# Kernel tuning notes

Hardware: AMD Instinct MI355X
Metric: run time of the kernel (lower is better)

Reference implementation:

```python
import jax, jax.numpy as jnp
import numpy as np
from jax import lax

K = 3          # kernel size
PAD = 1        # (K-1)//2
C = 64         # channels
RED = 16       # channel-attention reduction


def conv2d(x, w, b=None):
    # x [B,C,H,W], w [O,I,kh,kw]
    out = lax.conv_general_dilated(x, w, (1, 1), 'SAME',
                                   dimension_numbers=('NCHW', 'OIHW', 'NCHW'))
    if b is not None:
        out = out + b[None, :, None, None]
    return out


def rcab(x, w1, b1, w2, b2, caw1, cab1, caw2, cab2):
    res = conv2d(x, w1, b1)
    res = jax.nn.relu(res)
    res = conv2d(res, w2, b2)
    # channel attention: global avg pool -> 1x1 conv -> relu -> 1x1 conv -> sigmoid
    y = jnp.mean(res, axis=(2, 3), keepdims=True)
    y = jax.nn.relu(conv2d(y, caw1, cab1))
    y = jax.nn.sigmoid(conv2d(y, caw2, cab2))
    return res * y + x


def deform_conv(x, inter, fea, off_w, off_b, mask_w, mask_b, weight):
    # Modulated deformable conv: offsets/mask predicted from concat(inter, fea).
    B, Cc, H, W = x.shape
    KK = K * K
    guide = jnp.concatenate([inter, fea], axis=1)
    offset = conv2d(guide, off_w, off_b)                    # [B, 2*KK, H, W]
    mask = 2.0 * jax.nn.sigmoid(conv2d(guide, mask_w, mask_b))  # [B, KK, H, W]
    off = offset.reshape(B, KK, 2, H, W)
    oy, ox = off[:, :, 0], off[:, :, 1]                     # [B, KK, H, W]

    ky = (jnp.arange(KK) // K - PAD).astype(x.dtype)        # kernel tap y offsets
    kx = (jnp.arange(KK) % K - PAD).astype(x.dtype)
    ii = jnp.arange(H, dtype=x.dtype)[None, None, :, None]
    jj = jnp.arange(W, dtype=x.dtype)[None, None, None, :]
    ys = ii + ky[None, :, None, None] + oy                  # [B, KK, H, W]
    xs = jj + kx[None, :, None, None] + ox

    y0 = jnp.floor(ys); x0 = jnp.floor(xs)
    wy1 = ys - y0; wy0 = 1.0 - wy1
    wx1 = xs - x0; wx0 = 1.0 - wx1
    y0i = y0.astype(jnp.int32); x0i = x0.astype(jnp.int32)
    y1i = y0i + 1; x1i = x0i + 1

    x_flat = x.reshape(B, Cc, H * W)

    def gather(yi, xi):
        valid = ((yi >= 0) & (yi < H) & (xi >= 0) & (xi < W)).astype(x.dtype)
        idx = jnp.clip(yi, 0, H - 1) * W + jnp.clip(xi, 0, W - 1)   # [B,KK,H,W]
        idx = idx.reshape(B, KK * H * W)
        g = jax.vmap(lambda f, i: jnp.take(f, i, axis=1))(x_flat, idx)
        return g.reshape(B, Cc, KK, H, W) * valid[:, None]

    val = (gather(y0i, x0i) * (wy0 * wx0)[:, None]
           + gather(y0i, x1i) * (wy0 * wx1)[:, None]
           + gather(y1i, x0i) * (wy1 * wx0)[:, None]
           + gather(y1i, x1i) * (wy1 * wx1)[:, None])     # [B,C,KK,H,W]
    val = val * mask[:, None]
    w_flat = weight.reshape(weight.shape[0], Cc, KK)        # [O,I,KK]
    return jnp.einsum('bckhw,ock->bohw', val, w_flat)


def setup_inputs() -> dict:
    key = jax.random.key(0)
    ks = jax.random.split(key, 20)
    B, H, W = 4, 192, 192
    f32 = jnp.float32
    d = {
        'x':     jax.random.normal(ks[0], (B, C, H, W), f32),
        'inter': jax.random.normal(ks[1], (B, C, H, W), f32),
        'fea':   jax.random.normal(ks[2], (B, C, H, W), f32),
        # RCAB
        'rcab_w1': jax.random.normal(ks[3], (C, C, 3, 3), f32) * 0.05,
        'rcab_b1': jnp.zeros((C,), f32),
        'rcab_w2': jax.random.normal(ks[4], (C, C, 3, 3), f32) * 0.05,
        'rcab_b2': jnp.zeros((C,), f32),
        'ca_w1': jax.random.normal(ks[5], (C // RED, C, 1, 1), f32) * 0.05,
        'ca_b1': jnp.zeros((C // RED,), f32),
        'ca_w2': jax.random.normal(ks[6], (C, C // RED, 1, 1), f32) * 0.05,
        'ca_b2': jnp.zeros((C,), f32),
        # deformable conv offset/mask branch (input = concat(inter, fea) -> 2C)
        'off_w': jax.random.normal(ks[7], (2 * K * K, 2 * C, 3, 3), f32) * 0.01,
        'off_b': jnp.zeros((2 * K * K,), f32),
        'mask_w': jax.random.normal(ks[8], (K * K, 2 * C, 3, 3), f32) * 0.01,
        'mask_b': jnp.zeros((K * K,), f32),
        'deform_w': jax.random.normal(ks[9], (C, C, K, K), f32) * 0.05,
        # final conv
        'conv_w': jax.random.normal(ks[10], (C, C, 3, 3), f32) * 0.05,
        'conv_b': jnp.zeros((C,), f32),
    }
    return d


def reference(x, inter, fea, rcab_w1, rcab_b1, rcab_w2, rcab_b2,
              ca_w1, ca_b1, ca_w2, ca_b2,
              off_w, off_b, mask_w, mask_b, deform_w, conv_w, conv_b):
    out1 = rcab(x, rcab_w1, rcab_b1, rcab_w2, rcab_b2, ca_w1, ca_b1, ca_w2, ca_b2)
    out2 = deform_conv(out1, inter, fea, off_w, off_b, mask_w, mask_b, deform_w)
    return conv2d(out2 + out1, conv_w, conv_b)
```

## Files before the change

kernel.cpp:

```cpp
#include <hip/hip_runtime.h>
#include <hip/hip_bf16.h>
#include <hip/hip_fp16.h>
#include <math.h>

#define HSZ 192
#define WSZ 192
#define HWSZ (192*192)
#define PH 194
#define PP (PH*PH)
#define NB 4

typedef __attribute__((ext_vector_type(8))) short short8;
typedef __attribute__((ext_vector_type(4))) float f32x4;
typedef __attribute__((ext_vector_type(2))) float f32x2;

__device__ inline unsigned short f2bf(float f) { __hip_bfloat16 h = __float2bfloat16(f); return *(unsigned short*)&h; }
__device__ inline float bf2f(__hip_bfloat16 h) { return __bfloat162float(h); }
__device__ inline float bflo(unsigned u) { return __uint_as_float(u << 16); }
__device__ inline float bfhi(unsigned u) { return __uint_as_float(u & 0xffff0000u); }
__device__ inline f32x2 up2(unsigned u) {
  f32x2 r; r[0] = __uint_as_float(u << 16); r[1] = __uint_as_float(u & 0xffff0000u); return r;
}

#define GLDS(SRC, DST) __builtin_amdgcn_global_load_lds( \
    (const __attribute__((address_space(1))) unsigned int*)(const void*)(SRC), \
    (__attribute__((address_space(3))) unsigned int*)(void*)(DST), 16, 0, 0)

#define MFMA(A,B,C) __builtin_amdgcn_mfma_f32_16x16x32_bf16((A),(B),(C),0,0,0)

__global__ void zb2_k(__hip_bfloat16* xn, __hip_bfloat16* r1, __hip_bfloat16* out1,
                      __hip_bfloat16* cat) {
  int job = blockIdx.y;
  __hip_bfloat16* buf = job == 0 ? xn : job == 1 ? r1 : job == 2 ? out1 : cat;
  int Cn = (job == 3) ? 128 : 64;
  int cg8 = Cn >> 3;
  int tot = NB * 772 * cg8;
  int idx = blockIdx.x * 256 + threadIdx.x;
  if (idx >= tot) return;
  int cg = idx % cg8; int rem = idx / cg8;
  int e = rem % 772; int b = rem / 772;
  int h, w2;
  if (e < 194) { h = 0; w2 = e; }
  else if (e < 388) { h = 193; w2 = e - 194; }
  else if (e < 580) { h = e - 388 + 1; w2 = 0; }
  else { h = e - 580 + 1; w2 = 193; }
  uint4 z = make_uint4(0, 0, 0, 0);
  *(uint4*)&buf[(((size_t)b * PH + h) * PH + w2) * Cn + cg * 8] = z;
}

__global__ void wts_k(const float* __restrict__ rw1, const float* __restrict__ rw2,
                      const float* __restrict__ cw, const float* __restrict__ offw,
                      const float* __restrict__ maskw, const float* __restrict__ offb,
                      const float* __restrict__ maskb, const float* __restrict__ dwv,
                      short* wt1, short* wt2c, short* wtf, short* wtom, float* ob,
                      short* wtb, float* meanz) {
  int job = blockIdx.y;
  int idx = blockIdx.x * 256 + threadIdx.x;
  if (job < 3) {
    const float* src = job == 0 ? rw1 : job == 1 ? rw2 : cw;
    short* dst = job == 0 ? wt1 : job == 1 ? wt2c : wtf;
    int kk = idx >> 12, rem = idx & 4095;
    int co = rem >> 6, ci = rem & 63;
    dst[idx] = (short)f2bf(src[(co * 64 + ci) * 9 + kk]);
  } else if (job == 3) {
    int kk = idx >> 12, rem = idx & 4095;
    int co = rem >> 7, ci = rem & 127;
    float v = 0.f;
    if (co < 18) v = offw[(co * 128 + ci) * 9 + kk];
    else if (co < 27) v = maskw[((co - 18) * 128 + ci) * 9 + kk];
    wtom[idx] = (short)f2bf(v);
    if (idx < 32) ob[idx] = idx < 18 ? offb[idx] : (idx < 27 ? maskb[idx - 18] : 0.f);
  } else {
    int o = idx / 576, rem = idx - o * 576;
    int kk = rem >> 6, ci = rem & 63;
    wtb[idx] = (short)f2bf(dwv[(o * 64 + ci) * 9 + kk]);
    if (blockIdx.x == 0 && threadIdx.x < 256) meanz[threadIdx.x] = 0.f;
  }
}

__global__ __launch_bounds__(256) void cvt_k(const float* __restrict__ x,
    const float* __restrict__ inter, const float* __restrict__ fea,
    __hip_bfloat16* __restrict__ xn, __hip_bfloat16* __restrict__ cat) {
  int job = blockIdx.z;
  const float* src = job == 0 ? x : job == 1 ? inter : fea;
  __hip_bfloat16* dst = job == 0 ? xn : cat;
  int Cdst = job == 0 ? 64 : 128;
  int coff = job == 2 ? 64 : 0;
  __shared__ float s[64][65];
  int p0 = blockIdx.x * 64; int b = blockIdx.y;
  int lane = threadIdx.x & 63, g = threadIdx.x >> 6;
#pragma unroll
  for (int i = 0; i < 16; ++i) {
    int c = i * 4 + g;
    s[c][lane] = src[((size_t)b * 64 + c) * HWSZ + p0 + lane];
  }
  __syncthreads();
  int pix = threadIdx.x >> 2, cg = threadIdx.x & 3;
  int h = p0 / WSZ, w0 = p0 - h * WSZ + pix;
  size_t addr = (((size_t)b * PH + h + 1) * PH + 1 + w0) * Cdst + coff + cg * 16;
  unsigned pk2[8];
#pragma unroll
  for (int t = 0; t < 8; ++t)
    pk2[t] = (unsigned)f2bf(s[cg * 16 + 2 * t][pix]) | ((unsigned)f2bf(s[cg * 16 + 2 * t + 1][pix]) << 16);
  *(uint4*)&dst[addr]     = make_uint4(pk2[0], pk2[1], pk2[2], pk2[3]);
  *(uint4*)&dst[addr + 8] = make_uint4(pk2[4], pk2[5], pk2[6], pk2[7]);
}

template<int OUT_MODE, bool RELU, bool MEANACC>
__global__ __launch_bounds__(256, 2) void conv_mfma_k(
    const __hip_bfloat16* __restrict__ inp, const short* __restrict__ wt,
    const float* __restrict__ bias, __hip_bfloat16* __restrict__ outB,
    float* __restrict__ outF, float* __restrict__ meanout) {
  int flat = (blockIdx.x & 7) * 96 + (blockIdx.x >> 3);
  const int b = flat / 192, h = flat - (flat / 192) * 192;
  const int tid = threadIdx.x, lane = tid & 63, wid = tid >> 6;
  const int q = lane >> 4, r16 = lane & 15;
  __shared__ __align__(16) short tile[3 * 200 * 64];
  __shared__ float smean[4][64];

  {
    const char* gb = (const char*)(inp + ((size_t)b * PH + h) * (PH * 64));
    for (int s = wid; s < 75; s += 4) {
      int rr = s / 25, si = s - rr * 25;
      int pix = 8 * si + (lane >> 3);
      const char* src = gb + (size_t)rr * (PH * 128) + pix * 128
                      + ((((lane & 7) ^ ((lane >> 3) & 7))) << 4);
      GLDS(src, tile + rr * 12800 + si * 512);
    }
  }

  f32x4 acc[3][4];
  if (OUT_MODE == 0) {
#pragma unroll
    for (int nf = 0; nf < 4; ++nf) {
      float4 bv = *(const float4*)&bias[nf * 16 + q * 4];
      f32x4 v; v[0] = bv.x; v[1] = bv.y; v[2] = bv.z; v[3] = bv.w;
      acc[0][nf] = v; acc[1][nf] = v; acc[2][nf] = v;
    }
  } else {
#pragma unroll
    for (int nf = 0; nf < 4; ++nf) {
      float bs = bias[nf * 16 + r16];
      f32x4 v; v[0] = bs; v[1] = bs; v[2] = bs; v[3] = bs;
      acc[0][nf] = v; acc[1][nf] = v; acc[2][nf] = v;
    }
  }

  short8 bfr[2][2][4];
  {
    const short* wk0 = wt + r16 * 64 + q * 8;
#pragma unroll
    for (int nf = 0; nf < 4; ++nf) {
      bfr[0][0][nf] = *(const short8*)(wk0 + nf * 1024);
      bfr[0][1][nf] = *(const short8*)(wk0 + nf * 1024 + 32);
    }
  }
  __syncthreads();

  const int wm0 = wid * 48;
#pragma unroll
  for (int kk = 0; kk < 9; ++kk) {
    const int ky = kk / 3, kx = kk - ky * 3;
    const int cur = kk & 1;
    if (kk < 8) {
      const short* wk = wt + (kk + 1) * 4096 + r16 * 64 + q * 8;
#pragma unroll
      for (int nf = 0; nf < 4; ++nf) {
        bfr[cur ^ 1][0][nf] = *(const short8*)(wk + nf * 1024);
        bfr[cur ^ 1][1][nf] = *(const short8*)(wk + nf * 1024 + 32);
      }
    }
#pragma unroll
    for (int mf = 0; mf < 3; ++mf) {
      int pix = wm0 + mf * 16 + r16 + kx;
      const char* ab = (const char*)tile + ky * 25600 + pix * 128;
      int sw = (pix & 7) << 4;
      short8 a0 = *(const short8*)(ab + ((q << 4) ^ sw));
      short8 a1 = *(const short8*)(ab + (((q + 4) << 4) ^ sw));
#pragma unroll
      for (int nf = 0; nf < 4; ++nf) {
        if (OUT_MODE == 0) {
          acc[mf][nf] = MFMA(bfr[cur][0][nf], a0, acc[mf][nf]);
          acc[mf][nf] = MFMA(bfr[cur][1][nf], a1, acc[mf][nf]);
        } else {
          acc[mf][nf] = MFMA(a0, bfr[cur][0][nf], acc[mf][nf]);
          acc[mf][nf] = MFMA(a1, bfr[cur][1][nf], acc[mf][nf]);
        }
      }
    }
  }

  if (MEANACC) {
    float t[4][4];
#pragma unroll
    for (int nf = 0; nf < 4; ++nf)
#pragma unroll
      for (int rg = 0; rg < 4; ++rg)
        t[nf][rg] = acc[0][nf][rg] + acc[1][nf][rg] + acc[2][nf][rg];
#pragma unroll
    for (int m = 1; m < 16; m <<= 1)
#pragma unroll
      for (int nf = 0; nf < 4; ++nf)
#pragma unroll
        for (int rg = 0; rg < 4; ++rg)
          t[nf][rg] += __shfl_xor(t[nf][rg], m);
    if (r16 == 0)
#pragma unroll
      for (int nf = 0; nf < 4; ++nf)
#pragma unroll
        for (int rg = 0; rg < 4; ++rg)
          smean[wid][nf * 16 + q * 4 + rg] = t[nf][rg];
    __syncthreads();
    if (tid < 64)
      atomicAdd(&meanout[b * 64 + tid],
                (smean[0][tid] + smean[1][tid] + smean[2][tid] + smean[3][tid]) * (1.f / 36864.f));
  }

  if (OUT_MODE == 0) {
    __syncthreads();
#pragma unroll
    for (int mf = 0; mf < 3; ++mf)
#pragma unroll
      for (int nf = 0; nf < 4; ++nf) {
        f32x4 v = acc[mf][nf];
        if (RELU) { v[0] = fmaxf(v[0], 0.f); v[1] = fmaxf(v[1], 0.f); v[2] = fmaxf(v[2], 0.f); v[3] = fmaxf(v[3], 0.f); }
        unsigned lo = (unsigned)f2bf(v[0]) | ((unsigned)f2bf(v[1]) << 16);
        unsigned hi = (unsigned)f2bf(v[2]) | ((unsigned)f2bf(v[3]) << 16);
        int pix = wm0 + mf * 16 + r16;
        int byteoff = (pix * 128 + nf * 32 + q * 8) ^ ((pix & 7) << 4);
        *(uint2*)((char*)tile + byteoff) = make_uint2(lo, hi);
      }
    __syncthreads();
    char* orow = (char*)outB + ((((size_t)b * PH + h + 1) * PH + 1) * 64) * 2;
    for (int s = wid; s < 24; s += 4) {
      int pix = 8 * s + (lane >> 3);
      int g16 = ((lane & 7) ^ (pix & 7)) << 4;
      uint4 d = *(const uint4*)((const char*)tile + pix * 128 + g16);
      *(uint4*)(orow + pix * 128 + ((lane & 7) << 4)) = d;
    }
  } else {
    float* ob2 = outF + (size_t)b * 64 * HWSZ + h * WSZ;
#pragma unroll
    for (int mf = 0; mf < 3; ++mf)
#pragma unroll
      for (int nf = 0; nf < 4; ++nf) {
        int pix0 = wm0 + mf * 16 + q * 4;
        int co = nf * 16 + r16;
        *(f32x4*)&ob2[(size_t)co * HWSZ + pix0] = acc[mf][nf];
      }
  }
}

__global__ __launch_bounds__(256, 3) void offmask_mfma_k(
    const __hip_bfloat16* __restrict__ cat, const short* __restrict__ wt2,
    const float* __restrict__ ob, float* __restrict__ om) {
  const int h = blockIdx.x, b = blockIdx.y;
  const int tid = threadIdx.x, lane = tid & 63, wid = tid >> 6;
  const int q = lane >> 4, r16 = lane & 15;
  __shared__ __align__(16) short tile[200 * 128];

  f32x4 acc[3][2];
#pragma unroll
  for (int nf = 0; nf < 2; ++nf) {
    float bs = ob[nf * 16 + r16];
    f32x4 v; v[0] = bs; v[1] = bs; v[2] = bs; v[3] = bs;
    acc[0][nf] = v; acc[1][nf] = v; acc[2][nf] = v;
  }
  const char* gb = (const char*)(cat + ((size_t)b * PH + h) * (PH * 128));
  const int wm0 = wid * 48;

  short8 bfr[2][4][2];
  {
    const short* wk0 = wt2 + r16 * 128 + q * 8;
#pragma unroll
    for (int c4 = 0; c4 < 4; ++c4) {
      bfr[0][c4][0] = *(const short8*)(wk0 + c4 * 32);
      bfr[0][c4][1] = *(const short8*)(wk0 + 2048 + c4 * 32);
    }
  }

#pragma unroll
  for (int r = 0; r < 3; ++r) {
    __syncthreads();
    for (int s = wid; s < 50; s += 4) {
      int pix = 4 * s + (lane >> 4);
      const char* src = gb + (size_t)r * (PH * 256) + pix * 256
                      + ((((lane & 15) ^ (pix & 15))) << 4);
      GLDS(src, tile + s * 512);
    }
    __syncthreads();
#pragma unroll
    for (int kx = 0; kx < 3; ++kx) {
      const int kk = r * 3 + kx;
      const int cur = kk & 1;
      if (kk < 8) {
        const short* wk = wt2 + (kk + 1) * 4096 + r16 * 128 + q * 8;
#pragma unroll
        for (int c4 = 0; c4 < 4; ++c4) {
          bfr[cur ^ 1][c4][0] = *(const short8*)(wk + c4 * 32);
          bfr[cur ^ 1][c4][1] = *(const short8*)(wk + 2048 + c4 * 32);
        }
      }
#pragma unroll
      for (int mf = 0; mf < 3; ++mf) {
        int pix = wm0 + mf * 16 + r16 + kx;
        const char* ab = (const char*)tile + pix * 256;
        int sw = (pix & 15) << 4;
        short8 a0 = *(const short8*)(ab + ((q << 4) ^ sw));
        short8 a1 = *(const short8*)(ab + (((4 + q) << 4) ^ sw));
        short8 a2 = *(const short8*)(ab + (((8 + q) << 4) ^ sw));
        short8 a3 = *(const short8*)(ab + (((12 + q) << 4) ^ sw));
        acc[mf][0] = MFMA(a0, bfr[cur][0][0], acc[mf][0]); acc[mf][1] = MFMA(a0, bfr[cur][0][1], acc[mf][1]);
        acc[mf][0] = MFMA(a1, bfr[cur][1][0], acc[mf][0]); acc[mf][1] = MFMA(a1, bfr[cur][1][1], acc[mf][1]);
        acc[mf][0] = MFMA(a2, bfr[cur][2][0], acc[mf][0]); acc[mf][1] = MFMA(a2, bfr[cur][2][1], acc[mf][1]);
        acc[mf][0] = MFMA(a3, bfr[cur][3][0], acc[mf][0]); acc[mf][1] = MFMA(a3, bfr[cur][3][1], acc[mf][1]);
      }
    }
  }
#pragma unroll
  for (int mf = 0; mf < 3; ++mf)
#pragma unroll
    for (int nf = 0; nf < 2; ++nf) {
      int co = nf * 16 + r16;
      if (co < 27) {
        f32x4 v = acc[mf][nf];
        if (co >= 18) {
          v[0] = 2.f / (1.f + expf(-v[0])); v[1] = 2.f / (1.f + expf(-v[1]));
          v[2] = 2.f / (1.f + expf(-v[2])); v[3] = 2.f / (1.f + expf(-v[3]));
        }
        *(f32x4*)&om[((size_t)(b * 27 + co)) * HWSZ + h * WSZ + wm0 + mf * 16 + q * 4] = v;
      }
    }
}

__global__ __launch_bounds__(256) void out1_k(const __hip_bfloat16* __restrict__ res, const __hip_bfloat16* __restrict__ xn,
    const float* __restrict__ mean, const float* __restrict__ w1, const float* __restrict__ b1,
    const float* __restrict__ w2, const float* __restrict__ b2,
    __hip_bfloat16* __restrict__ out1) {
  int idx = blockIdx.x * 256 + threadIdx.x;
  int b = idx / 294912; int rem = idx - b * 294912;
  int p = rem >> 3, c8 = rem & 7;
  int lane = threadIdx.x & 63, wid = threadIdx.x >> 6;

  __shared__ float s_t[4];
  {
    float prod = w1[wid * 64 + lane] * mean[b * 64 + lane];
#pragma unroll
    for (int m = 1; m < 64; m <<= 1) prod += __shfl_xor(prod, m);
    if (lane == 0) s_t[wid] = fmaxf(prod + b1[wid], 0.f);
  }
  __syncthreads();
  float t0 = s_t[0], t1 = s_t[1], t2 = s_t[2], t3 = s_t[3];

  int hh = p / WSZ, ww = p - hh * WSZ;
  size_t off = ((size_t)b * PP + (size_t)(hh + 1) * PH + ww + 1) * 64 + c8 * 8;
  const __hip_bfloat16* rp = res + off;
  const __hip_bfloat16* xp = xn + off;
  __hip_bfloat16* op = out1 + off;
  unsigned pk[4];
#pragma unroll
  for (int t = 0; t < 4; ++t) {
    float y0, y1;
    {
      int c = c8 * 8 + 2 * t;
      const float4 wv0 = *(const float4*)&w2[c * 4];
      const float4 wv1 = *(const float4*)&w2[(c + 1) * 4];
      float v0 = b2[c]     + wv0.x * t0 + wv0.y * t1 + wv0.z * t2 + wv0.w * t3;
      float v1 = b2[c + 1] + wv1.x * t0 + wv1.y * t1 + wv1.z * t2 + wv1.w * t3;
      y0 = 1.f / (1.f + expf(-v0));
      y1 = 1.f / (1.f + expf(-v1));
    }
    float o0 = bf2f(rp[2 * t]) * y0 + bf2f(xp[2 * t]);
    float o1 = bf2f(rp[2 * t + 1]) * y1 + bf2f(xp[2 * t + 1]);
    pk[t] = (unsigned)f2bf(o0) | ((unsigned)f2bf(o1) << 16);
  }
  *(uint4*)op = make_uint4(pk[0], pk[1], pk[2], pk[3]);
}

__global__ __launch_bounds__(256) void deform_mfma_k(
    const __hip_bfloat16* __restrict__ nhwc, const float* __restrict__ om,
    const short* __restrict__ wtb, __hip_bfloat16* __restrict__ fin) {
  int blk = (blockIdx.x & 7) * 576 + (blockIdx.x >> 3);
  int b = blk / 1152;
  int p0 = (blk - b * 1152) * 32;
  int tid = threadIdx.x, lane = tid & 63, wid = tid >> 6;
  int q = lane >> 4, r16 = lane & 15;
  __shared__ __align__(16) short sA[2][32][64];
  __shared__ __half2 s_bw[2][9][32];
  __shared__ int s_pk[9][32];

  const float* omb = om + (size_t)b * 27 * HWSZ + p0;
  for (int e = tid; e < 288; e += 256) {
    int kk = e >> 5, pix = e & 31;
    int p = p0 + pix;
    int h = p / WSZ, w2 = p - h * WSZ;
    float oy = omb[(size_t)(2 * kk) * HWSZ + pix];
    float ox = omb[(size_t)(2 * kk + 1) * HWSZ + pix];
    float m2 = omb[(size_t)(18 + kk) * HWSZ + pix];
    float ys = (float)(h + kk / 3 - 1) + oy;
    float xs = (float)(w2 + kk % 3 - 1) + ox;
    float y0f = floorf(ys), x0f = floorf(xs);
    float wy1 = ys - y0f, wx1 = xs - x0f;
    float wy0 = 1.f - wy1, wx0 = 1.f - wx1;
    int y0 = (int)y0f, x0i = (int)x0f;
    int y1 = y0 + 1, x1 = x0i + 1;
    float vy0 = (y0 >= 0 && y0 < HSZ) ? 1.f : 0.f;
    float vx0 = (x0i >= 0 && x0i < WSZ) ? 1.f : 0.f;
    float vy1 = (y1 >= 0 && y1 < HSZ) ? 1.f : 0.f;
    float vx1 = (x1 >= 0 && x1 < WSZ) ? 1.f : 0.f;
    int y0c = min(max(y0, 0), HSZ - 1), x0c = min(max(x0i, 0), WSZ - 1);
    int y1c = min(max(y1, 0), HSZ - 1), x1c = min(max(x1, 0), WSZ - 1);
    s_bw[0][kk][pix] = __floats2half2_rn(wy0 * wx0 * m2 * vy0 * vx0, wy0 * wx1 * m2 * vy0 * vx1);
    s_bw[1][kk][pix] = __floats2half2_rn(wy1 * wx0 * m2 * vy1 * vx0, wy1 * wx1 * m2 * vy1 * vx1);
    s_pk[kk][pix] = ((((y0c + 1) * PH) + x0c + 1) << 2) | ((y1c - y0c) << 1) | (x1c - x0c);
  }
  __syncthreads();

  const __hip_bfloat16* nb = nhwc + (size_t)b * PP * 64;
  const int spix = tid >> 3, lg = tid & 7;
  const int swz = (spix & 7) << 4;
  const int rsw = (r16 & 7) << 4;

  uint4 A0, B0, C0, D0, A1, B1, C1, D1, A2, B2, C2, D2;
  float2 wab0, wcd0, wab1, wcd1, wab2, wcd2;

#define ISSUE_R(KK, Av, Bv, Cv, Dv, Wab, Wcd) do { \
    Wab = __half22float2(s_bw[0][KK][spix]); \
    Wcd = __half22float2(s_bw[1][KK][spix]); \
    int pk_ = s_pk[KK][spix]; \
    int i00_ = pk_ >> 2, dy_ = (pk_ >> 1) & 1, dx_ = pk_ & 1; \
    const __hip_bfloat16* g_ = nb + (size_t)i00_ * 64 + lg * 8; \
    Av = *(const uint4*)g_; \
    Bv = *(const uint4*)(g_ + dx_ * 64); \
    Cv = *(const uint4*)(g_ + dy_ * (PH * 64)); \
    Dv = *(const uint4*)(g_ + (dy_ * PH + dx_) * 64); \
  } while (0)
#define CSTORE_R(BUFOFF, Av, Bv, Cv, Dv, Wab, Wcd) do { \
    const unsigned* ap_ = (const unsigned*)&Av; const unsigned* bp_ = (const unsigned*)&Bv; \
    const unsigned* cp_ = (const unsigned*)&Cv; const unsigned* dp_ = (const unsigned*)&Dv; \
    unsigned o_[4]; \
    _Pragma("unroll") \
    for (int j_ = 0; j_ < 4; ++j_) { \
      f32x2 v_ = up2(ap_[j_]) * Wab.x + up2(bp_[j_]) * Wab.y + up2(cp_[j_]) * Wcd.x + up2(dp_[j_]) * Wcd.y; \
      asm("v_cvt_pk_bf16_f32 %0, %1, %2" : "=v"(o_[j_]) : "v"(v_[0]), "v"(v_[1])); \
    } \
    *(uint4*)((char*)sA + (BUFOFF) + spix * 128 + ((lg * 16) ^ swz)) = make_uint4(o_[0], o_[1], o_[2], o_[3]); \
  } while (0)

  ISSUE_R(0, A0, B0, C0, D0, wab0, wcd0);
  CSTORE_R(0, A0, B0, C0, D0, wab0, wcd0);
  ISSUE_R(1, A0, B0, C0, D0, wab0, wcd0);
  ISSUE_R(2, A1, B1, C1, D1, wab1, wcd1);
  ISSUE_R(3, A2, B2, C2, D2, wab2, wcd2);

  f32x4 acc0 = (f32x4){0.f, 0.f, 0.f, 0.f};
  f32x4 acc1 = (f32x4){0.f, 0.f, 0.f, 0.f};
  const short* wrow = wtb + (size_t)(wid * 16 + r16) * 576;
  const char* a0base = (const char*)sA + r16 * 128;
  const char* a1base = (const char*)sA + (r16 + 16) * 128;

#pragma unroll
  for (int kk = 0; kk < 9; ++kk) {
    const int bo = (kk & 1) * 4096;
    __syncthreads();
    __builtin_amdgcn_s_setprio(1);
#pragma unroll
    for (int s = 0; s < 2; ++s) {
      short8 wf = *(const short8*)(wrow + kk * 64 + s * 32 + q * 8);
      int off = bo + ((s * 64 + q * 16) ^ rsw);
      short8 va = *(const short8*)(a0base + off);
      short8 vb = *(const short8*)(a1base + off);
      acc0 = MFMA(wf, va, acc0);
      acc1 = MFMA(wf, vb, acc1);
    }
    __builtin_amdgcn_s_setprio(0);
    if (kk < 8) {
      const int nbo = ((kk + 1) & 1) * 4096;
      const int rs = kk % 3;
      if (rs == 0) {
        CSTORE_R(nbo, A0, B0, C0, D0, wab0, wcd0);
        if (kk + 4 <= 8) ISSUE_R(kk + 4, A0, B0, C0, D0, wab0, wcd0);
      } else if (rs == 1) {
        CSTORE_R(nbo, A1, B1, C1, D1, wab1, wcd1);
        if (kk + 4 <= 8) ISSUE_R(kk + 4, A1, B1, C1, D1, wab1, wcd1);
      } else {
        CSTORE_R(nbo, A2, B2, C2, D2, wab2, wcd2);
        if (kk + 4 <= 8) ISSUE_R(kk + 4, A2, B2, C2, D2, wab2, wcd2);
      }
    }
  }

  int h0 = p0 / WSZ, w0 = p0 - h0 * WSZ;
  size_t ro = ((size_t)(h0 + 1) * PH + w0 + 1) * 64;
  const __hip_bfloat16* resid = nb + ro;
  __hip_bfloat16* fp = fin + (size_t)b * PP * 64 + ro;
#pragma unroll
  for (int nf = 0; nf < 2; ++nf) {
    f32x4 av = nf ? acc1 : acc0;
    int pix = r16 + nf * 16;
    int co = wid * 16 + q * 4;
    const unsigned* rr = (const unsigned*)(resid + (size_t)pix * 64 + co);
    unsigned r0 = rr[0], r1 = rr[1];
    float o0 = av[0] + bflo(r0);
    float o1 = av[1] + bfhi(r0);
    float o2 = av[2] + bflo(r1);
    float o3 = av[3] + bfhi(r1);
    uint2 pk2 = make_uint2((unsigned)f2bf(o0) | ((unsigned)f2bf(o1) << 16),
                           (unsigned)f2bf(o2) | ((unsigned)f2bf(o3) << 16));
    *(uint2*)(fp + (size_t)pix * 64 + co) = pk2;
  }
#undef ISSUE_R
#undef CSTORE_R
}

extern "C" void kernel_launch(void* const* d_in, const int* in_sizes, int n_in,
                              void* d_out, int out_size, void* d_ws, size_t ws_size,
                              hipStream_t stream) {
  (void)in_sizes; (void)n_in; (void)out_size; (void)ws_size;
  const float* x     = (const float*)d_in[0];
  const float* inter = (const float*)d_in[1];
  const float* fea   = (const float*)d_in[2];
  const float* rw1   = (const float*)d_in[3];
  const float* rb1   = (const float*)d_in[4];
  const float* rw2   = (const float*)d_in[5];
  const float* rb2   = (const float*)d_in[6];
  const float* caw1  = (const float*)d_in[7];
  const float* cab1  = (const float*)d_in[8];
  const float* caw2  = (const float*)d_in[9];
  const float* cab2  = (const float*)d_in[10];
  const float* offw  = (const float*)d_in[11];
  const float* offb  = (const float*)d_in[12];
  const float* maskw = (const float*)d_in[13];
  const float* maskb = (const float*)d_in[14];
  const float* dw    = (const float*)d_in[15];
  const float* cw    = (const float*)d_in[16];
  const float* cb    = (const float*)d_in[17];

  char* w = (char*)d_ws;
  const size_t P64 = (size_t)NB * PP * 64 * 2 + 4096;
  const size_t PCAT = (size_t)NB * PP * 128 * 2 + 4096;
  __hip_bfloat16* xn   = (__hip_bfloat16*)(w);
  __hip_bfloat16* r1   = (__hip_bfloat16*)(w + P64);
  __hip_bfloat16* res  = (__hip_bfloat16*)(w + 2 * P64);
  __hip_bfloat16* out1 = (__hip_bfloat16*)(w + 3 * P64);
  __hip_bfloat16* cat  = (__hip_bfloat16*)(w + 4 * P64);
  char* tail = w + 4 * P64 + PCAT;
  short* wt1  = (short*)tail; tail += 73728;
  short* wt2c = (short*)tail; tail += 73728;
  short* wtf  = (short*)tail; tail += 73728;
  short* wtom = (short*)tail; tail += 73728;
  float* obb  = (float*)tail; tail += 128;
  short* wtb  = (short*)tail; tail += 73728;
  float* mean = (float*)tail; tail += 1024;
  float* omb  = (float*)res;
  __hip_bfloat16* fin = r1;

  zb2_k<<<dim3(194, 4), 256, 0, stream>>>(xn, r1, out1, cat);
  wts_k<<<dim3(144, 5), 256, 0, stream>>>(rw1, rw2, cw, offw, maskw, offb, maskb, dw,
                                          wt1, wt2c, wtf, wtom, obb, wtb, mean);
  cvt_k<<<dim3(576, 4, 3), 256, 0, stream>>>(x, inter, fea, xn, cat);

  conv_mfma_k<0, true , false><<<768, 256, 0, stream>>>(xn, wt1, rb1, r1, nullptr, nullptr);
  conv_mfma_k<0, false, true ><<<768, 256, 0, stream>>>(r1, wt2c, rb2, res, nullptr, mean);
  out1_k<<<4608, 256, 0, stream>>>(res, xn, mean, caw1, cab1, caw2, cab2, out1);
  offmask_mfma_k<<<dim3(192, 4), 256, 0, stream>>>(cat, wtom, obb, omb);
  deform_mfma_k<<<NB * 1152, 256, 0, stream>>>(out1, omb, wtb, fin);
  conv_mfma_k<1, false, false><<<768, 256, 0, stream>>>(fin, wtf, cb, nullptr, (float*)d_out, nullptr);
}
```

Before: 272.5 us.

## Double-buffer conv input rows in LDS and raise conv occupancy

The 3x3 conv kernel now stages one padded input row at a time into two ping-pong LDS buffers instead of loading all three rows up front. It loads the next row while MFMAs run on the current one. This cuts LDS per block from three rows to two, so launch bounds rise from 2 to 3 blocks per CU, at the cost of an extra barrier per kernel row. In the deformable kernel, the packed f32x2 bilinear blend with inline-asm bf16 packing is replaced by scalar FMAs and software bf16 conversion, and the s_setprio hints around the MFMAs are removed. These deformable-kernel edits may add ALU work and lose scheduling priority.

```diff
diff --git a/kernel.cpp b/kernel.cpp
--- a/kernel.cpp
+++ b/kernel.cpp
@@ -12,15 +12,11 @@
 
 typedef __attribute__((ext_vector_type(8))) short short8;
 typedef __attribute__((ext_vector_type(4))) float f32x4;
-typedef __attribute__((ext_vector_type(2))) float f32x2;
 
 __device__ inline unsigned short f2bf(float f) { __hip_bfloat16 h = __float2bfloat16(f); return *(unsigned short*)&h; }
 __device__ inline float bf2f(__hip_bfloat16 h) { return __bfloat162float(h); }
 __device__ inline float bflo(unsigned u) { return __uint_as_float(u << 16); }
 __device__ inline float bfhi(unsigned u) { return __uint_as_float(u & 0xffff0000u); }
-__device__ inline f32x2 up2(unsigned u) {
-  f32x2 r; r[0] = __uint_as_float(u << 16); r[1] = __uint_as_float(u & 0xffff0000u); return r;
-}
 
 #define GLDS(SRC, DST) __builtin_amdgcn_global_load_lds( \
     (const __attribute__((address_space(1))) unsigned int*)(const void*)(SRC), \
@@ -107,7 +103,7 @@
 }
 
 template<int OUT_MODE, bool RELU, bool MEANACC>
-__global__ __launch_bounds__(256, 2) void conv_mfma_k(
+__global__ __launch_bounds__(256, 3) void conv_mfma_k(
     const __hip_bfloat16* __restrict__ inp, const short* __restrict__ wt,
     const float* __restrict__ bias, __hip_bfloat16* __restrict__ outB,
     float* __restrict__ outF, float* __restrict__ meanout) {
@@ -115,19 +111,20 @@
   const int b = flat / 192, h = flat - (flat / 192) * 192;
   const int tid = threadIdx.x, lane = tid & 63, wid = tid >> 6;
   const int q = lane >> 4, r16 = lane & 15;
-  __shared__ __align__(16) short tile[3 * 200 * 64];
+  __shared__ __align__(16) short tile[2][200 * 64];
   __shared__ float smean[4][64];
 
-  {
-    const char* gb = (const char*)(inp + ((size_t)b * PH + h) * (PH * 64));
-    for (int s = wid; s < 75; s += 4) {
-      int rr = s / 25, si = s - rr * 25;
-      int pix = 8 * si + (lane >> 3);
-      const char* src = gb + (size_t)rr * (PH * 128) + pix * 128
-                      + ((((lane & 7) ^ ((lane >> 3) & 7))) << 4);
-      GLDS(src, tile + rr * 12800 + si * 512);
-    }
-  }
+  const __hip_bfloat16* base = inp + ((size_t)b * PH + h) * (PH * 64);
+#define STAGE(BUF, R) do { \
+    const char* gb_ = (const char*)(base + (size_t)(R) * (PH * 64)); \
+    for (int s_ = wid; s_ < 25; s_ += 4) { \
+      int pix_ = 8 * s_ + (lane >> 3); \
+      const char* src_ = gb_ + pix_ * 128 + ((((lane & 7) ^ ((lane >> 3) & 7))) << 4); \
+      GLDS(src_, tile[BUF] + s_ * 512); \
+    } \
+  } while (0)
+
+  STAGE(0, 0);
 
   f32x4 acc[3][4];
   if (OUT_MODE == 0) {
@@ -159,36 +156,43 @@
 
   const int wm0 = wid * 48;
 #pragma unroll
-  for (int kk = 0; kk < 9; ++kk) {
-    const int ky = kk / 3, kx = kk - ky * 3;
-    const int cur = kk & 1;
-    if (kk < 8) {
-      const short* wk = wt + (kk + 1) * 4096 + r16 * 64 + q * 8;
-#pragma unroll
-      for (int nf = 0; nf < 4; ++nf) {
-        bfr[cur ^ 1][0][nf] = *(const short8*)(wk + nf * 1024);
-        bfr[cur ^ 1][1][nf] = *(const short8*)(wk + nf * 1024 + 32);
-      }
-    }
-#pragma unroll
-    for (int mf = 0; mf < 3; ++mf) {
-      int pix = wm0 + mf * 16 + r16 + kx;
-      const char* ab = (const char*)tile + ky * 25600 + pix * 128;
-      int sw = (pix & 7) << 4;
-      short8 a0 = *(const short8*)(ab + ((q << 4) ^ sw));
-      short8 a1 = *(const short8*)(ab + (((q + 4) << 4) ^ sw));
-#pragma unroll
-      for (int nf = 0; nf < 4; ++nf) {
-        if (OUT_MODE == 0) {
-          acc[mf][nf] = MFMA(bfr[cur][0][nf], a0, acc[mf][nf]);
-          acc[mf][nf] = MFMA(bfr[cur][1][nf], a1, acc[mf][nf]);
-        } else {
-          acc[mf][nf] = MFMA(a0, bfr[cur][0][nf], acc[mf][nf]);
-          acc[mf][nf] = MFMA(a1, bfr[cur][1][nf], acc[mf][nf]);
+  for (int ky = 0; ky < 3; ++ky) {
+    const int cb = ky & 1;
+    if (ky < 2) STAGE(cb ^ 1, ky + 1);
+#pragma unroll
+    for (int kx = 0; kx < 3; ++kx) {
+      const int kk = ky * 3 + kx;
+      const int cur = kk & 1;
+      if (kk < 8) {
+        const short* wk = wt + (kk + 1) * 4096 + r16 * 64 + q * 8;
+#pragma unroll
+        for (int nf = 0; nf < 4; ++nf) {
+          bfr[cur ^ 1][0][nf] = *(const short8*)(wk + nf * 1024);
+          bfr[cur ^ 1][1][nf] = *(const short8*)(wk + nf * 1024 + 32);
         }
       }
-    }
-  }
+#pragma unroll
+      for (int mf = 0; mf < 3; ++mf) {
+        int pix = wm0 + mf * 16 + r16 + kx;
+        const char* ab = (const char*)tile[cb] + pix * 128;
+        int sw = (pix & 7) << 4;
+        short8 a0 = *(const short8*)(ab + ((q << 4) ^ sw));
+        short8 a1 = *(const short8*)(ab + (((q + 4) << 4) ^ sw));
+#pragma unroll
+        for (int nf = 0; nf < 4; ++nf) {
+          if (OUT_MODE == 0) {
+            acc[mf][nf] = MFMA(bfr[cur][0][nf], a0, acc[mf][nf]);
+            acc[mf][nf] = MFMA(bfr[cur][1][nf], a1, acc[mf][nf]);
+          } else {
+            acc[mf][nf] = MFMA(a0, bfr[cur][0][nf], acc[mf][nf]);
+            acc[mf][nf] = MFMA(a1, bfr[cur][1][nf], acc[mf][nf]);
+          }
+        }
+      }
+    }
+    __syncthreads();
+  }
+#undef STAGE
 
   if (MEANACC) {
     float t[4][4];
@@ -217,7 +221,6 @@
   }
 
   if (OUT_MODE == 0) {
-    __syncthreads();
 #pragma unroll
     for (int mf = 0; mf < 3; ++mf)
 #pragma unroll
@@ -228,14 +231,14 @@
         unsigned hi = (unsigned)f2bf(v[2]) | ((unsigned)f2bf(v[3]) << 16);
         int pix = wm0 + mf * 16 + r16;
         int byteoff = (pix * 128 + nf * 32 + q * 8) ^ ((pix & 7) << 4);
-        *(uint2*)((char*)tile + byteoff) = make_uint2(lo, hi);
+        *(uint2*)((char*)tile[1] + byteoff) = make_uint2(lo, hi);
       }
     __syncthreads();
     char* orow = (char*)outB + ((((size_t)b * PH + h + 1) * PH + 1) * 64) * 2;
     for (int s = wid; s < 24; s += 4) {
       int pix = 8 * s + (lane >> 3);
       int g16 = ((lane & 7) ^ (pix & 7)) << 4;
-      uint4 d = *(const uint4*)((const char*)tile + pix * 128 + g16);
+      uint4 d = *(const uint4*)((const char*)tile[1] + pix * 128 + g16);
       *(uint4*)(orow + pix * 128 + ((lane & 7) << 4)) = d;
     }
   } else {
@@ -441,8 +444,9 @@
     unsigned o_[4]; \
     _Pragma("unroll") \
     for (int j_ = 0; j_ < 4; ++j_) { \
-      f32x2 v_ = up2(ap_[j_]) * Wab.x + up2(bp_[j_]) * Wab.y + up2(cp_[j_]) * Wcd.x + up2(dp_[j_]) * Wcd.y; \
-      asm("v_cvt_pk_bf16_f32 %0, %1, %2" : "=v"(o_[j_]) : "v"(v_[0]), "v"(v_[1])); \
+      float lo_ = Wab.x * bflo(ap_[j_]) + Wab.y * bflo(bp_[j_]) + Wcd.x * bflo(cp_[j_]) + Wcd.y * bflo(dp_[j_]); \
+      float hi_ = Wab.x * bfhi(ap_[j_]) + Wab.y * bfhi(bp_[j_]) + Wcd.x * bfhi(cp_[j_]) + Wcd.y * bfhi(dp_[j_]); \
+      o_[j_] = (unsigned)f2bf(lo_) | ((unsigned)f2bf(hi_) << 16); \
     } \
     *(uint4*)((char*)sA + (BUFOFF) + spix * 128 + ((lg * 16) ^ swz)) = make_uint4(o_[0], o_[1], o_[2], o_[3]); \
   } while (0)
@@ -463,7 +467,6 @@
   for (int kk = 0; kk < 9; ++kk) {
     const int bo = (kk & 1) * 4096;
     __syncthreads();
-    __builtin_amdgcn_s_setprio(1);
 #pragma unroll
     for (int s = 0; s < 2; ++s) {
       short8 wf = *(const short8*)(wrow + kk * 64 + s * 32 + q * 8);
@@ -473,7 +476,6 @@
       acc0 = MFMA(wf, va, acc0);
       acc1 = MFMA(wf, vb, acc1);
     }
-    __builtin_amdgcn_s_setprio(0);
     if (kk < 8) {
       const int nbo = ((kk + 1) & 1) * 4096;
       const int rs = kk % 3;
```

New measurement: 268.7 us. About the same (-1.4%).
